# Performance work log

Hardware: AMD Instinct MI355X
Metric: run time of the kernel (lower is better)

## Reference

```python
import jax, jax.numpy as jnp
from jax import lax
import numpy as np

B, NW, L, E, H, V = 8192, 4, 16, 128, 128, 64  # batch, words/example, max chars, emsize, hidden, char vocab


def setup_inputs() -> dict:
    key = jax.random.key(0)
    ks = jax.random.split(key, 13)
    s = 0.05
    return {
        "word_ids": jax.random.randint(ks[0], (B, NW, L), 0, V, dtype=jnp.int32),
        "lengths": jax.random.randint(ks[1], (B, NW), 1, L + 1, dtype=jnp.int32),
        "emb_i": jax.random.normal(ks[2], (V, E), jnp.float32),
        "W_ih": jax.random.normal(ks[3], (4 * H, E), jnp.float32) * s,
        "W_hh": jax.random.normal(ks[4], (4 * H, H), jnp.float32) * s,
        "b_ih": jax.random.normal(ks[5], (4 * H,), jnp.float32) * s,
        "b_hh": jax.random.normal(ks[6], (4 * H,), jnp.float32) * s,
        "conv1_w": jax.random.normal(ks[7], (4, 1, 2, 2), jnp.float32) * 0.5,
        "conv1_b": jax.random.normal(ks[8], (4,), jnp.float32) * 0.1,
        "conv2_w": jax.random.normal(ks[9], (8, 4, 2, 2), jnp.float32) * 0.5,
        "conv2_b": jax.random.normal(ks[10], (8,), jnp.float32) * 0.1,
        "scorer_w": jax.random.normal(ks[11], (1, 2 * 2 * 8), jnp.float32) * 0.2,
        "scorer_b": jax.random.normal(ks[12], (1,), jnp.float32) * 0.1,
    }


def reference(word_ids, lengths, emb_i, W_ih, W_hh, b_ih, b_hh,
              conv1_w, conv1_b, conv2_w, conv2_b, scorer_w, scorer_b):
    Bx, NWx, Lx = word_ids.shape
    Hh = W_hh.shape[1]
    BN = Bx * NWx
    # char embeddings for all words, packed: [L, BN, E]
    xs = emb_i[word_ids.reshape(BN, Lx)].transpose(1, 0, 2)
    # ragged lengths -> per-step update mask [L, BN]
    mask = jnp.arange(Lx, dtype=lengths.dtype)[:, None] < lengths.reshape(-1)[None, :]
    h0 = jnp.zeros((BN, Hh), emb_i.dtype)

    def step(carry, xm):
        h, c = carry
        x_t, m = xm
        gates = x_t @ W_ih.T + b_ih + h @ W_hh.T + b_hh  # torch LSTMCell gate order i,f,g,o
        i, f, g, o = jnp.split(gates, 4, axis=-1)
        i = jax.nn.sigmoid(i); f = jax.nn.sigmoid(f)
        g = jnp.tanh(g); o = jax.nn.sigmoid(o)
        c_new = f * c + i * g
        h_new = o * jnp.tanh(c_new)
        m = m[:, None]
        return (jnp.where(m, h_new, h), jnp.where(m, c_new, c)), None

    (h, c), _ = lax.scan(step, (h0, h0), (xs, mask))
    # Model.encode returns the cell state c
    reps = c.reshape(Bx, NWx, Hh)

    # pairwise cosine similarity matrix [B, NW, NW]
    norms = jnp.sqrt(jnp.sum(reps * reps, axis=-1))
    dots = jnp.einsum('bih,bjh->bij', reps, reps)
    cos = dots / (norms[:, :, None] * norms[:, None, :])

    # tiny 2-layer CNN scorer on the NWxNW matrix (NCHW)
    dn = ('NCHW', 'OIHW', 'NCHW')
    x_img = cos[:, None, :, :]
    out = jax.nn.relu(lax.conv_general_dilated(x_img, conv1_w, (1, 1), 'VALID', dimension_numbers=dn)
                      + conv1_b[None, :, None, None])
    out = jax.nn.relu(lax.conv_general_dilated(out, conv2_w, (1, 1), 'VALID', dimension_numbers=dn)
                      + conv2_b[None, :, None, None])
    flat = out.reshape(Bx, -1)  # channel-major flatten matches torch .view
    score = flat @ scorer_w.T + scorer_b
    return jax.nn.sigmoid(score)  # [B, 1] discriminator prob
```

## Files before the change

### kernel.cpp

```cpp
#include <hip/hip_runtime.h>

#define BSZ    8192
#define NWRD   4
#define SEQL   16
#define HDIM   128
#define NSEQ   (BSZ * NWRD)
#define WGSEQ  32
#define UPB    80
#define BINCAP (UPB * WGSEQ)
#define NUNITS (16 * UPB)
#define HSTRIDE 136

typedef float  f32x4  __attribute__((ext_vector_type(4)));
typedef float  f32x16 __attribute__((ext_vector_type(16)));
typedef __bf16 bf16x8 __attribute__((ext_vector_type(8)));

union AccU { f32x16 v; f32x4 q[4]; float f[16]; };
union HPack { unsigned short s[4]; unsigned long long u64; };

__device__ __forceinline__ unsigned short f2bf(float f) {
    unsigned int u = __builtin_bit_cast(unsigned int, f);
    return (unsigned short)((u + 0x7fff + ((u >> 16) & 1)) >> 16);
}
__device__ __forceinline__ float sigm(float x) {
    return __builtin_amdgcn_rcpf(1.f + __builtin_amdgcn_exp2f(x * -1.44269504f));
}
__device__ __forceinline__ float tanhx(float x) {
    return 1.f - 2.f * __builtin_amdgcn_rcpf(1.f + __builtin_amdgcn_exp2f(x * 2.88539008f));
}

__global__ void prep4(const float* __restrict__ emb, const float* __restrict__ W_ih,
                      const float* __restrict__ b_ih, const float* __restrict__ b_hh,
                      const float* __restrict__ W_hh, const int* __restrict__ lengths,
                      float* __restrict__ P2T, unsigned short* __restrict__ WA,
                      int* __restrict__ perm, int* __restrict__ gh)
{
    __shared__ int lh[16], gbase[16];
    const int blk = blockIdx.x, tid = threadIdx.x;

    if (blk < 128) {
        int idx = blk * 256 + tid;
        int v = idx >> 9, g = (idx >> 7) & 3, j = idx & 127;
        int n = g * 128 + j;
        float s = b_ih[n] + b_hh[n];
        const float* er = emb  + v * 128;
        const float* wr = W_ih + n * 128;
        for (int e = 0; e < 128; e += 4)
            s += er[e]*wr[e] + er[e+1]*wr[e+1] + er[e+2]*wr[e+2] + er[e+3]*wr[e+3];
        P2T[idx] = s;
    } else if (blk < 384) {
        int idx = (blk - 128) * 256 + tid;
        int jj = idx & 7, lane = (idx >> 3) & 63, kc = (idx >> 9) & 7, tt = idx >> 12;
        int wv = tt >> 2, g = tt & 3;
        int n = g * 128 + wv * 32 + (lane & 31);
        int k = kc * 16 + (lane >> 5) * 8 + jj;
        WA[idx] = f2bf(W_hh[n * 128 + k]);
    } else {
        if (tid < 16) lh[tid] = 0;
        __syncthreads();
        int i = (blk - 384) * 256 + tid;
        int b = 16 - lengths[i];
        int rank = atomicAdd(&lh[b], 1);
        __syncthreads();
        if (tid < 16) gbase[tid] = atomicAdd(&gh[tid], lh[tid]);
        __syncthreads();
        perm[b * BINCAP + gbase[b] + rank] = i;
    }
}

__global__ __launch_bounds__(256, 2) void lstm4(
    const int* __restrict__ word_ids, const int* __restrict__ perm,
    const int* __restrict__ gh, const float* __restrict__ P2T,
    const unsigned short* __restrict__ WA, float* __restrict__ c_out)
{
    __shared__ __align__(16) unsigned short hbuf[2][WGSEQ * HSTRIDE];
    __shared__ int words_s[WGSEQ * 17];
    __shared__ int sid_s[WGSEQ];

    const int tid    = threadIdx.x;
    const int wv     = tid >> 6;
    const int lane   = tid & 63;
    const int lane31 = lane & 31;
    const int hl     = lane >> 5;

    const int u    = blockIdx.x;
    const int b    = u / UPB;
    const int widx = u % UPB;
    const int cnt  = gh[b];
    const int ml   = (widx * WGSEQ < cnt) ? (16 - b) : 0;

    bf16x8 afr[4][8];
#pragma unroll
    for (int g = 0; g < 4; ++g)
#pragma unroll
        for (int kc = 0; kc < 8; ++kc)
            afr[g][kc] = *(const bf16x8*)(WA + (((wv * 4 + g) * 8 + kc) * 64 + lane) * 8);

    if (tid < WGSEQ) {
        int slot = widx * WGSEQ + tid;
        sid_s[tid] = (slot < cnt) ? perm[b * BINCAP + slot] : 0;
    }
    for (int i = tid; i < WGSEQ * HSTRIDE; i += 256) ((int*)hbuf)[i] = 0;
    __syncthreads();
    for (int i = tid; i < WGSEQ * SEQL; i += 256)
        words_s[(i >> 4) * 17 + (i & 15)] = word_ids[sid_s[i >> 4] * SEQL + (i & 15)];
    __syncthreads();

    if (ml > 0) {
        f32x4 cq[4] = {{0,0,0,0},{0,0,0,0},{0,0,0,0},{0,0,0,0}};
        const char* P2c  = (const char*)P2T;
        const int pboff  = wv * 128 + hl * 16;
        const int rdo    = lane31 * HSTRIDE;
        const int jbase  = wv * 32 + 4 * hl;

#pragma unroll 1
        for (int t = 0; t < ml; ++t) {
            const unsigned short* __restrict__ hr = hbuf[t & 1];
            unsigned short*       __restrict__ hw = hbuf[(t + 1) & 1];

            const int w = words_s[lane31 * 17 + t];
            const char* pb = P2c + ((size_t)w << 11) + pboff;
            AccU acc[4];
#pragma unroll
            for (int g = 0; g < 4; ++g)
#pragma unroll
                for (int q = 0; q < 4; ++q)
                    acc[g].q[q] = *(const f32x4*)(pb + g * 512 + q * 32);

            bf16x8 bf[8];
#pragma unroll
            for (int kc = 0; kc < 8; ++kc)
                bf[kc] = *(const bf16x8*)(hr + rdo + kc * 16 + hl * 8);

#pragma unroll
            for (int kc = 0; kc < 8; ++kc) {
                const bf16x8 bb = bf[kc];
#pragma unroll
                for (int g = 0; g < 4; ++g)
                    acc[g].v = __builtin_amdgcn_mfma_f32_32x32x16_bf16(afr[g][kc], bb, acc[g].v, 0, 0, 0);
            }

#pragma unroll
            for (int q = 0; q < 4; ++q) {
                HPack hp;
#pragma unroll
                for (int d = 0; d < 4; ++d) {
                    const int r = q * 4 + d;
                    float ig = sigm(acc[0].f[r]);
                    float fg = sigm(acc[1].f[r]);
                    float gg = tanhx(acc[2].f[r]);
                    float og = sigm(acc[3].f[r]);
                    float cn = fg * cq[q][d] + ig * gg;
                    cq[q][d] = cn;
                    hp.s[d] = f2bf(og * tanhx(cn));
                }
                *(unsigned long long*)(hw + rdo + jbase + 8 * q) = hp.u64;
            }
            __syncthreads();
        }

        if (widx * WGSEQ + lane31 < cnt) {
            const int sid = sid_s[lane31];
#pragma unroll
            for (int q = 0; q < 4; ++q)
                *(f32x4*)(c_out + sid * HDIM + jbase + 8 * q) = cq[q];
        }
    }
}

__global__ __launch_bounds__(256) void epilogue(
    const float* __restrict__ c_ws,
    const float* __restrict__ conv1_w, const float* __restrict__ conv1_b,
    const float* __restrict__ conv2_w, const float* __restrict__ conv2_b,
    const float* __restrict__ scorer_w, const float* __restrict__ scorer_b,
    float* __restrict__ out)
{
    __shared__ __align__(16) float reps[8 * NWRD * HDIM];
    __shared__ float gram_s[8 * 16];

    const int tid = threadIdx.x;
    const int b0  = blockIdx.x * 8;

    for (int i = tid; i < 8 * NWRD * HDIM; i += 256)
        reps[i] = c_ws[b0 * NWRD * HDIM + i];
    __syncthreads();

    const int bt  = tid >> 5;
    const int sub = tid & 31;

    float dval = 0.f;
    if (sub < 16) {
        int i = sub >> 2, j = sub & 3;
        const f32x4* ci = (const f32x4*)(reps + (bt * 4 + i) * HDIM);
        const f32x4* cj = (const f32x4*)(reps + (bt * 4 + j) * HDIM);
        f32x4 s4 = {0.f, 0.f, 0.f, 0.f};
        for (int k = 0; k < HDIM / 4; ++k) s4 += ci[k] * cj[k];
        dval = s4.x + s4.y + s4.z + s4.w;
        gram_s[bt * 16 + sub] = dval;
    }
    __syncthreads();
    float cosv = 0.f;
    if (sub < 16) {
        int i = sub >> 2, j = sub & 3;
        float di = gram_s[bt * 16 + i * 4 + i];
        float dj = gram_s[bt * 16 + j * 4 + j];
        cosv = __fdividef(dval, sqrtf(di * dj));
    }
    __syncthreads();
    if (sub < 16) gram_s[bt * 16 + sub] = cosv;
    __syncthreads();

    if (sub == 0) {
        float img[4][4];
#pragma unroll
        for (int i = 0; i < 4; ++i)
#pragma unroll
            for (int j = 0; j < 4; ++j) img[i][j] = gram_s[bt * 16 + i * 4 + j];

        float o1[4][3][3];
#pragma unroll
        for (int ch = 0; ch < 4; ++ch) {
            float w00 = conv1_w[ch*4+0], w01 = conv1_w[ch*4+1];
            float w10 = conv1_w[ch*4+2], w11 = conv1_w[ch*4+3];
            float bb  = conv1_b[ch];
#pragma unroll
            for (int y = 0; y < 3; ++y)
#pragma unroll
                for (int x = 0; x < 3; ++x) {
                    float s = bb + w00*img[y][x]   + w01*img[y][x+1]
                                 + w10*img[y+1][x] + w11*img[y+1][x+1];
                    o1[ch][y][x] = s > 0.f ? s : 0.f;
                }
        }
        float sc = scorer_b[0];
#pragma unroll
        for (int oc = 0; oc < 8; ++oc) {
            float bb = conv2_b[oc];
#pragma unroll
            for (int y = 0; y < 2; ++y)
#pragma unroll
                for (int x = 0; x < 2; ++x) {
                    float s = bb;
#pragma unroll
                    for (int ic = 0; ic < 4; ++ic) {
                        const float* w = conv2_w + oc * 16 + ic * 4;
                        s += w[0]*o1[ic][y][x]   + w[1]*o1[ic][y][x+1]
                           + w[2]*o1[ic][y+1][x] + w[3]*o1[ic][y+1][x+1];
                    }
                    float rl = s > 0.f ? s : 0.f;
                    sc += rl * scorer_w[oc * 4 + y * 2 + x];
                }
        }
        out[blockIdx.x * 8 + bt] = sigm(sc);
    }
}

extern "C" void kernel_launch(void* const* d_in, const int* in_sizes, int n_in,
                              void* d_out, int out_size, void* d_ws, size_t ws_size,
                              hipStream_t stream)
{
    const int*   word_ids = (const int*)d_in[0];
    const int*   lengths  = (const int*)d_in[1];
    const float* emb      = (const float*)d_in[2];
    const float* W_ih     = (const float*)d_in[3];
    const float* W_hh     = (const float*)d_in[4];
    const float* b_ih     = (const float*)d_in[5];
    const float* b_hh     = (const float*)d_in[6];
    const float* conv1_w  = (const float*)d_in[7];
    const float* conv1_b  = (const float*)d_in[8];
    const float* conv2_w  = (const float*)d_in[9];
    const float* conv2_b  = (const float*)d_in[10];
    const float* scorer_w = (const float*)d_in[11];
    const float* scorer_b = (const float*)d_in[12];
    float* out = (float*)d_out;

    char* ws = (char*)d_ws;
    float*          P2T  = (float*)(ws + 0);
    unsigned short* WA   = (unsigned short*)(ws + (128<<10));
    int*            perm = (int*)(ws + (256<<10));
    int*            gh   = (int*)(ws + (416<<10));
    float*          c_ws = (float*)(ws + (512<<10));

    hipMemsetAsync(gh, 0, 16 * sizeof(int), stream);
    prep4   <<<512,   256, 0, stream>>>(emb, W_ih, b_ih, b_hh, W_hh, lengths,
                                        P2T, WA, perm, gh);
    lstm4   <<<NUNITS, 256, 0, stream>>>(word_ids, perm, gh, P2T, WA, c_ws);
    epilogue<<<BSZ / 8, 256, 0, stream>>>(c_ws, conv1_w, conv1_b, conv2_w, conv2_b,
                                          scorer_w, scorer_b, out);
}
```

Measured before the change: 197.0 us.

## Peel first LSTM step, prefetch next-step input gates, skip dead work

The LSTM loop is restructured. Step 0 skips the MFMA because h is zero, so the hbuf zeroing goes away. The next step's precomputed input-gate loads are issued right after each h slice is written, so their latency overlaps the barrier. The last step skips the output gate and the h write. Empty blocks now exit early before loading the weight fragments, bf16 packing uses the hardware v_cvt_pk_bf16_f32 instruction, and the prep dot product is vectorized.

```diff
diff --git a/kernel.cpp b/kernel.cpp
--- a/kernel.cpp
+++ b/kernel.cpp
@@ -16,7 +16,6 @@
 typedef __bf16 bf16x8 __attribute__((ext_vector_type(8)));
 
 union AccU { f32x16 v; f32x4 q[4]; float f[16]; };
-union HPack { unsigned short s[4]; unsigned long long u64; };
 
 __device__ __forceinline__ unsigned short f2bf(float f) {
     unsigned int u = __builtin_bit_cast(unsigned int, f);
@@ -42,12 +41,12 @@
         int idx = blk * 256 + tid;
         int v = idx >> 9, g = (idx >> 7) & 3, j = idx & 127;
         int n = g * 128 + j;
-        float s = b_ih[n] + b_hh[n];
-        const float* er = emb  + v * 128;
-        const float* wr = W_ih + n * 128;
-        for (int e = 0; e < 128; e += 4)
-            s += er[e]*wr[e] + er[e+1]*wr[e+1] + er[e+2]*wr[e+2] + er[e+3]*wr[e+3];
-        P2T[idx] = s;
+        const f32x4* er = (const f32x4*)(emb  + v * 128);
+        const f32x4* wr = (const f32x4*)(W_ih + n * 128);
+        f32x4 s4 = er[0] * wr[0];
+#pragma unroll
+        for (int e = 1; e < 32; ++e) s4 += er[e] * wr[e];
+        P2T[idx] = s4.x + s4.y + s4.z + s4.w + b_ih[n] + b_hh[n];
     } else if (blk < 384) {
         int idx = (blk - 128) * 256 + tid;
         int jj = idx & 7, lane = (idx >> 3) & 63, kc = (idx >> 9) & 7, tt = idx >> 12;
@@ -68,6 +67,64 @@
     }
 }
 
+
+#define GATE_PHASE(T, WRITE)                                                    \
+    {                                                                           \
+        const int wr_ = (WRITE);                                                \
+        unsigned short* hw_ = hbuf[((T) + 1) & 1];                              \
+        int wn_ = 0;                                                            \
+        if (wr_) wn_ = words_s[lane31 * 17 + (T) + 1];                          \
+        const char* pbn_ = P2c + ((size_t)wn_ << 11) + pboff;                   \
+        _Pragma("unroll")                                                       \
+        for (int q = 0; q < 4; ++q) {                                           \
+            float hv_[4];                                                       \
+            _Pragma("unroll")                                                   \
+            for (int d = 0; d < 4; ++d) {                                       \
+                const int r = q * 4 + d;                                        \
+                float ig = sigm(acc[0].f[r]);                                   \
+                float fg = sigm(acc[1].f[r]);                                   \
+                float gg = tanhx(acc[2].f[r]);                                  \
+                float cn = fg * cq[q][d] + ig * gg;                             \
+                cq[q][d] = cn;                                                  \
+                if (wr_) {                                                      \
+                    float og = sigm(acc[3].f[r]);                               \
+                    hv_[d] = og * tanhx(cn);                                    \
+                }                                                               \
+            }                                                                   \
+            if (wr_) {                                                          \
+                unsigned int plo_, phi_;                                        \
+                asm("v_cvt_pk_bf16_f32 %0, %1, %2"                              \
+                    : "=v"(plo_) : "v"(hv_[0]), "v"(hv_[1]));                   \
+                asm("v_cvt_pk_bf16_f32 %0, %1, %2"                              \
+                    : "=v"(phi_) : "v"(hv_[2]), "v"(hv_[3]));                   \
+                unsigned long long pu_ =                                        \
+                    ((unsigned long long)phi_ << 32) | plo_;                    \
+                *(unsigned long long*)(hw_ + rdo + jbase + 8 * q) = pu_;        \
+                             \
+                _Pragma("unroll")                                               \
+                for (int g = 0; g < 4; ++g)                                     \
+                    acc[g].q[q] = *(const f32x4*)(pbn_ + g * 512 + q * 32);     \
+            }                                                                   \
+        }                                                                       \
+    }
+
+#define MFMA_STEP(T)                                                            \
+    {                                                                           \
+        const unsigned short* hr_ = hbuf[(T) & 1];                              \
+        bf16x8 bfv_[8];                                                         \
+        _Pragma("unroll")                                                       \
+        for (int kc = 0; kc < 8; ++kc)                                          \
+            bfv_[kc] = *(const bf16x8*)(hr_ + rdo + kc * 16 + hl * 8);          \
+        _Pragma("unroll")                                                       \
+        for (int kc = 0; kc < 8; ++kc) {                                        \
+            const bf16x8 bb_ = bfv_[kc];                                        \
+            _Pragma("unroll")                                                   \
+            for (int g = 0; g < 4; ++g)                                         \
+                acc[g].v = __builtin_amdgcn_mfma_f32_32x32x16_bf16(             \
+                    afr[g][kc], bb_, acc[g].v, 0, 0, 0);                        \
+        }                                                                       \
+    }
+
 __global__ __launch_bounds__(256, 2) void lstm4(
     const int* __restrict__ word_ids, const int* __restrict__ perm,
     const int* __restrict__ gh, const float* __restrict__ P2T,
@@ -87,84 +144,60 @@
     const int b    = u / UPB;
     const int widx = u % UPB;
     const int cnt  = gh[b];
-    const int ml   = (widx * WGSEQ < cnt) ? (16 - b) : 0;
-
-    bf16x8 afr[4][8];
-#pragma unroll
-    for (int g = 0; g < 4; ++g)
-#pragma unroll
-        for (int kc = 0; kc < 8; ++kc)
-            afr[g][kc] = *(const bf16x8*)(WA + (((wv * 4 + g) * 8 + kc) * 64 + lane) * 8);
+    if (widx * WGSEQ >= cnt) return;
+    const int ml   = 16 - b;
 
     if (tid < WGSEQ) {
         int slot = widx * WGSEQ + tid;
         sid_s[tid] = (slot < cnt) ? perm[b * BINCAP + slot] : 0;
     }
-    for (int i = tid; i < WGSEQ * HSTRIDE; i += 256) ((int*)hbuf)[i] = 0;
     __syncthreads();
     for (int i = tid; i < WGSEQ * SEQL; i += 256)
         words_s[(i >> 4) * 17 + (i & 15)] = word_ids[sid_s[i >> 4] * SEQL + (i & 15)];
     __syncthreads();
 
-    if (ml > 0) {
-        f32x4 cq[4] = {{0,0,0,0},{0,0,0,0},{0,0,0,0},{0,0,0,0}};
-        const char* P2c  = (const char*)P2T;
-        const int pboff  = wv * 128 + hl * 16;
-        const int rdo    = lane31 * HSTRIDE;
-        const int jbase  = wv * 32 + 4 * hl;
-
+    bf16x8 afr[4][8];
+#pragma unroll
+    for (int g = 0; g < 4; ++g)
+#pragma unroll
+        for (int kc = 0; kc < 8; ++kc)
+            afr[g][kc] = *(const bf16x8*)(WA + (((wv * 4 + g) * 8 + kc) * 64 + lane) * 8);
+
+    f32x4 cq[4] = {{0,0,0,0},{0,0,0,0},{0,0,0,0},{0,0,0,0}};
+    const char* P2c  = (const char*)P2T;
+    const int pboff  = wv * 128 + hl * 16;
+    const int rdo    = lane31 * HSTRIDE;
+    const int jbase  = wv * 32 + 4 * hl;
+
+    AccU acc[4];
+    {
+        const int w0 = words_s[lane31 * 17];
+        const char* pb = P2c + ((size_t)w0 << 11) + pboff;
+#pragma unroll
+        for (int g = 0; g < 4; ++g)
+#pragma unroll
+            for (int q = 0; q < 4; ++q)
+                acc[g].q[q] = *(const f32x4*)(pb + g * 512 + q * 32);
+    }
+
+    GATE_PHASE(0, ml > 1);
+    if (ml > 1) {
+        __syncthreads();
 #pragma unroll 1
-        for (int t = 0; t < ml; ++t) {
-            const unsigned short* __restrict__ hr = hbuf[t & 1];
-            unsigned short*       __restrict__ hw = hbuf[(t + 1) & 1];
-
-            const int w = words_s[lane31 * 17 + t];
-            const char* pb = P2c + ((size_t)w << 11) + pboff;
-            AccU acc[4];
-#pragma unroll
-            for (int g = 0; g < 4; ++g)
-#pragma unroll
-                for (int q = 0; q < 4; ++q)
-                    acc[g].q[q] = *(const f32x4*)(pb + g * 512 + q * 32);
-
-            bf16x8 bf[8];
-#pragma unroll
-            for (int kc = 0; kc < 8; ++kc)
-                bf[kc] = *(const bf16x8*)(hr + rdo + kc * 16 + hl * 8);
-
-#pragma unroll
-            for (int kc = 0; kc < 8; ++kc) {
-                const bf16x8 bb = bf[kc];
-#pragma unroll
-                for (int g = 0; g < 4; ++g)
-                    acc[g].v = __builtin_amdgcn_mfma_f32_32x32x16_bf16(afr[g][kc], bb, acc[g].v, 0, 0, 0);
-            }
-
-#pragma unroll
-            for (int q = 0; q < 4; ++q) {
-                HPack hp;
-#pragma unroll
-                for (int d = 0; d < 4; ++d) {
-                    const int r = q * 4 + d;
-                    float ig = sigm(acc[0].f[r]);
-                    float fg = sigm(acc[1].f[r]);
-                    float gg = tanhx(acc[2].f[r]);
-                    float og = sigm(acc[3].f[r]);
-                    float cn = fg * cq[q][d] + ig * gg;
-                    cq[q][d] = cn;
-                    hp.s[d] = f2bf(og * tanhx(cn));
-                }
-                *(unsigned long long*)(hw + rdo + jbase + 8 * q) = hp.u64;
-            }
+        for (int t = 1; t < ml - 1; ++t) {
+            MFMA_STEP(t);
+            GATE_PHASE(t, 1);
             __syncthreads();
         }
-
-        if (widx * WGSEQ + lane31 < cnt) {
-            const int sid = sid_s[lane31];
-#pragma unroll
-            for (int q = 0; q < 4; ++q)
-                *(f32x4*)(c_out + sid * HDIM + jbase + 8 * q) = cq[q];
-        }
+        MFMA_STEP(ml - 1);
+        GATE_PHASE(ml - 1, 0);
+    }
+
+    if (widx * WGSEQ + lane31 < cnt) {
+        const int sid = sid_s[lane31];
+#pragma unroll
+        for (int q = 0; q < 4; ++q)
+            *(f32x4*)(c_out + sid * HDIM + jbase + 8 * q) = cq[q];
     }
 }
 
```

After: 194.0 us. No clear change (-1.5%).

## Stage fp16 input-projection table in LDS and streamline LSTM recurrence step

Applied to the files above, without the earlier changes.

The precomputed embedding×W_ih projection table is now stored in fp16 with a swizzled layout and bulk-copied into LDS per workgroup with global_load_lds, replacing per-step global reads of the fp32 table. Word ids are packed into registers, the h buffer uses an XOR swizzle instead of padding, the first step skips the recurrent MFMA, the last step skips the h computation, and the gate math merges sigmoid/tanh reciprocals. Empty workgroups exit early. This trades a 64KB LDS footprint per block, which may lower occupancy, and fp16 rounding of the gate pre-activations for fewer global loads and less transcendental work.

```diff
diff --git a/kernel.cpp b/kernel.cpp
--- a/kernel.cpp
+++ b/kernel.cpp
@@ -4,19 +4,23 @@
 #define NWRD   4
 #define SEQL   16
 #define HDIM   128
+#define VOCAB  64
 #define NSEQ   (BSZ * NWRD)
 #define WGSEQ  32
 #define UPB    80
 #define BINCAP (UPB * WGSEQ)
 #define NUNITS (16 * UPB)
-#define HSTRIDE 136
-
-typedef float  f32x4  __attribute__((ext_vector_type(4)));
-typedef float  f32x16 __attribute__((ext_vector_type(16)));
-typedef __bf16 bf16x8 __attribute__((ext_vector_type(8)));
+
+#define AS1 __attribute__((address_space(1)))
+#define AS3 __attribute__((address_space(3)))
+
+typedef float    f32x4  __attribute__((ext_vector_type(4)));
+typedef float    f32x16 __attribute__((ext_vector_type(16)));
+typedef __bf16   bf16x8 __attribute__((ext_vector_type(8)));
+typedef _Float16 f16x8  __attribute__((ext_vector_type(8)));
+typedef int      i32x4  __attribute__((ext_vector_type(4)));
 
 union AccU { f32x16 v; f32x4 q[4]; float f[16]; };
-union HPack { unsigned short s[4]; unsigned long long u64; };
 
 __device__ __forceinline__ unsigned short f2bf(float f) {
     unsigned int u = __builtin_bit_cast(unsigned int, f);
@@ -25,14 +29,11 @@
 __device__ __forceinline__ float sigm(float x) {
     return __builtin_amdgcn_rcpf(1.f + __builtin_amdgcn_exp2f(x * -1.44269504f));
 }
-__device__ __forceinline__ float tanhx(float x) {
-    return 1.f - 2.f * __builtin_amdgcn_rcpf(1.f + __builtin_amdgcn_exp2f(x * 2.88539008f));
-}
 
 __global__ void prep4(const float* __restrict__ emb, const float* __restrict__ W_ih,
                       const float* __restrict__ b_ih, const float* __restrict__ b_hh,
                       const float* __restrict__ W_hh, const int* __restrict__ lengths,
-                      float* __restrict__ P2T, unsigned short* __restrict__ WA,
+                      unsigned short* __restrict__ P2H, unsigned short* __restrict__ WA,
                       int* __restrict__ perm, int* __restrict__ gh)
 {
     __shared__ int lh[16], gbase[16];
@@ -42,12 +43,17 @@
         int idx = blk * 256 + tid;
         int v = idx >> 9, g = (idx >> 7) & 3, j = idx & 127;
         int n = g * 128 + j;
-        float s = b_ih[n] + b_hh[n];
-        const float* er = emb  + v * 128;
-        const float* wr = W_ih + n * 128;
-        for (int e = 0; e < 128; e += 4)
-            s += er[e]*wr[e] + er[e+1]*wr[e+1] + er[e+2]*wr[e+2] + er[e+3]*wr[e+3];
-        P2T[idx] = s;
+        const f32x4* er = (const f32x4*)(emb  + v * 128);
+        const f32x4* wr = (const f32x4*)(W_ih + n * 128);
+        f32x4 s4 = er[0] * wr[0];
+#pragma unroll
+        for (int e = 1; e < 32; ++e) s4 += er[e] * wr[e];
+        float s = s4.x + s4.y + s4.z + s4.w + b_ih[n] + b_hh[n];
+        int wv = j >> 5, jr = j & 31;
+        int d = jr & 3, hl = (jr >> 2) & 1, q = jr >> 3;
+        int cc = g * 16 + wv * 4 + hl * 2 + (q >> 1);
+        int F  = v * 512 + ((cc ^ (v & 7)) << 3) + (q & 1) * 4 + d;
+        P2H[F] = __builtin_bit_cast(unsigned short, (_Float16)s);
     } else if (blk < 384) {
         int idx = (blk - 128) * 256 + tid;
         int jj = idx & 7, lane = (idx >> 3) & 63, kc = (idx >> 9) & 7, tt = idx >> 12;
@@ -70,12 +76,11 @@
 
 __global__ __launch_bounds__(256, 2) void lstm4(
     const int* __restrict__ word_ids, const int* __restrict__ perm,
-    const int* __restrict__ gh, const float* __restrict__ P2T,
+    const int* __restrict__ gh, const unsigned short* __restrict__ P2H,
     const unsigned short* __restrict__ WA, float* __restrict__ c_out)
 {
-    __shared__ __align__(16) unsigned short hbuf[2][WGSEQ * HSTRIDE];
-    __shared__ int words_s[WGSEQ * 17];
-    __shared__ int sid_s[WGSEQ];
+    __shared__ __align__(16) unsigned short ptab[VOCAB * 512];
+    __shared__ __align__(16) unsigned short hbuf[2][WGSEQ * 128];
 
     const int tid    = threadIdx.x;
     const int wv     = tid >> 6;
@@ -87,7 +92,20 @@
     const int b    = u / UPB;
     const int widx = u % UPB;
     const int cnt  = gh[b];
-    const int ml   = (widx * WGSEQ < cnt) ? (16 - b) : 0;
+    if (widx * WGSEQ >= cnt) return;
+    const int ml   = 16 - b;
+
+    {
+        const char* src = (const char*)P2H;
+        char*       dst = (char*)ptab;
+#pragma unroll
+        for (int r = 0; r < 16; ++r) {
+            const int off = r * 4096 + wv * 1024;
+            __builtin_amdgcn_global_load_lds(
+                (const AS1 unsigned int*)(src + off + lane * 16),
+                (AS3 unsigned int*)(dst + off), 16, 0, 0);
+        }
+    }
 
     bf16x8 afr[4][8];
 #pragma unroll
@@ -96,75 +114,108 @@
         for (int kc = 0; kc < 8; ++kc)
             afr[g][kc] = *(const bf16x8*)(WA + (((wv * 4 + g) * 8 + kc) * 64 + lane) * 8);
 
-    if (tid < WGSEQ) {
-        int slot = widx * WGSEQ + tid;
-        sid_s[tid] = (slot < cnt) ? perm[b * BINCAP + slot] : 0;
-    }
-    for (int i = tid; i < WGSEQ * HSTRIDE; i += 256) ((int*)hbuf)[i] = 0;
-    __syncthreads();
-    for (int i = tid; i < WGSEQ * SEQL; i += 256)
-        words_s[(i >> 4) * 17 + (i & 15)] = word_ids[sid_s[i >> 4] * SEQL + (i & 15)];
-    __syncthreads();
-
-    if (ml > 0) {
-        f32x4 cq[4] = {{0,0,0,0},{0,0,0,0},{0,0,0,0},{0,0,0,0}};
-        const char* P2c  = (const char*)P2T;
-        const int pboff  = wv * 128 + hl * 16;
-        const int rdo    = lane31 * HSTRIDE;
-        const int jbase  = wv * 32 + 4 * hl;
+    const int slot = widx * WGSEQ + lane31;
+    const int live = slot < cnt;
+    const int sid  = live ? perm[b * BINCAP + slot] : 0;
+    unsigned long long u0, u1;
+    {
+        const i32x4* wp = (const i32x4*)(word_ids + sid * SEQL);
+        i32x4 a = wp[0], b4 = wp[1], c4 = wp[2], d4 = wp[3];
+        unsigned lo0 = (unsigned)(a.x  | (a.y  << 8) | (a.z  << 16) | (a.w  << 24));
+        unsigned hi0 = (unsigned)(b4.x | (b4.y << 8) | (b4.z << 16) | (b4.w << 24));
+        unsigned lo1 = (unsigned)(c4.x | (c4.y << 8) | (c4.z << 16) | (c4.w << 24));
+        unsigned hi1 = (unsigned)(d4.x | (d4.y << 8) | (d4.z << 16) | (d4.w << 24));
+        u0 = ((unsigned long long)hi0 << 32) | lo0;
+        u1 = ((unsigned long long)hi1 << 32) | lo1;
+    }
+    __syncthreads();
+
+    f32x4 cq[4] = {{0,0,0,0},{0,0,0,0},{0,0,0,0},{0,0,0,0}};
+    const int      rdo_b = lane31 * 256;
+    const unsigned xv    = (unsigned)((lane31 & 7) << 4);
+    const int      jbase = wv * 32 + 4 * hl;
+    const int      ccb   = wv * 4 + hl * 2;
 
 #pragma unroll 1
-        for (int t = 0; t < ml; ++t) {
-            const unsigned short* __restrict__ hr = hbuf[t & 1];
-            unsigned short*       __restrict__ hw = hbuf[(t + 1) & 1];
-
-            const int w = words_s[lane31 * 17 + t];
-            const char* pb = P2c + ((size_t)w << 11) + pboff;
-            AccU acc[4];
+    for (int t = 0; t < ml; ++t) {
+        const int w = (int)(u0 & 63);
+        u0 = (u0 >> 8) | (u1 << 56); u1 >>= 8;
+
+        AccU acc[4];
+        {
+            const char*    rowp = (const char*)ptab + (w << 10);
+            const unsigned wx   = (unsigned)((w & 7) << 4);
 #pragma unroll
             for (int g = 0; g < 4; ++g)
 #pragma unroll
-                for (int q = 0; q < 4; ++q)
-                    acc[g].q[q] = *(const f32x4*)(pb + g * 512 + q * 32);
-
-            bf16x8 bf[8];
+                for (int s = 0; s < 2; ++s) {
+                    const unsigned off = ((unsigned)((g * 16 + ccb + s) << 4)) ^ wx;
+                    f16x8 hv = *(const f16x8*)(rowp + off);
+#pragma unroll
+                    for (int k = 0; k < 8; ++k)
+                        acc[g].f[s * 8 + k] = (float)hv[k];
+                }
+        }
+
+        if (t > 0) {
+            const char* hr = (const char*)hbuf[t & 1];
+            bf16x8 bfv[8];
 #pragma unroll
             for (int kc = 0; kc < 8; ++kc)
-                bf[kc] = *(const bf16x8*)(hr + rdo + kc * 16 + hl * 8);
-
+                bfv[kc] = *(const bf16x8*)(hr + rdo_b +
+                              (((unsigned)(kc * 32 + hl * 16)) ^ xv));
 #pragma unroll
             for (int kc = 0; kc < 8; ++kc) {
-                const bf16x8 bb = bf[kc];
+                const bf16x8 bb = bfv[kc];
 #pragma unroll
                 for (int g = 0; g < 4; ++g)
-                    acc[g].v = __builtin_amdgcn_mfma_f32_32x32x16_bf16(afr[g][kc], bb, acc[g].v, 0, 0, 0);
+                    acc[g].v = __builtin_amdgcn_mfma_f32_32x32x16_bf16(
+                        afr[g][kc], bb, acc[g].v, 0, 0, 0);
             }
-
-#pragma unroll
-            for (int q = 0; q < 4; ++q) {
-                HPack hp;
-#pragma unroll
-                for (int d = 0; d < 4; ++d) {
-                    const int r = q * 4 + d;
-                    float ig = sigm(acc[0].f[r]);
-                    float fg = sigm(acc[1].f[r]);
-                    float gg = tanhx(acc[2].f[r]);
-                    float og = sigm(acc[3].f[r]);
-                    float cn = fg * cq[q][d] + ig * gg;
-                    cq[q][d] = cn;
-                    hp.s[d] = f2bf(og * tanhx(cn));
+        }
+
+        const int wr = (t < ml - 1);
+        char* hw = (char*)hbuf[(t + 1) & 1];
+#pragma unroll
+        for (int q = 0; q < 4; ++q) {
+            float hv4[4];
+#pragma unroll
+            for (int d = 0; d < 4; ++d) {
+                const int r = q * 4 + d;
+                float ei = __builtin_amdgcn_exp2f(acc[0].f[r] * -1.44269504f);
+                float ef = __builtin_amdgcn_exp2f(acc[1].f[r] * -1.44269504f);
+                float eg = __builtin_amdgcn_exp2f(acc[2].f[r] *  2.88539008f);
+                float fg  = __builtin_amdgcn_rcpf(1.f + ef);
+                float igg = (eg - 1.f) *
+                            __builtin_amdgcn_rcpf((1.f + ei) * (1.f + eg));
+                float cn = cq[q][d] * fg + igg;
+                cq[q][d] = cn;
+                if (wr) {
+                    float eo = __builtin_amdgcn_exp2f(acc[3].f[r] * -1.44269504f);
+                    float ec = __builtin_amdgcn_exp2f(cn * 2.88539008f);
+                    hv4[d] = (ec - 1.f) *
+                             __builtin_amdgcn_rcpf((1.f + eo) * (1.f + ec));
                 }
-                *(unsigned long long*)(hw + rdo + jbase + 8 * q) = hp.u64;
             }
-            __syncthreads();
-        }
-
-        if (widx * WGSEQ + lane31 < cnt) {
-            const int sid = sid_s[lane31];
-#pragma unroll
-            for (int q = 0; q < 4; ++q)
-                *(f32x4*)(c_out + sid * HDIM + jbase + 8 * q) = cq[q];
-        }
+            if (wr) {
+                unsigned int plo_, phi_;
+                asm("v_cvt_pk_bf16_f32 %0, %1, %2"
+                    : "=v"(plo_) : "v"(hv4[0]), "v"(hv4[1]));
+                asm("v_cvt_pk_bf16_f32 %0, %1, %2"
+                    : "=v"(phi_) : "v"(hv4[2]), "v"(hv4[3]));
+                unsigned long long pu_ =
+                    ((unsigned long long)phi_ << 32) | plo_;
+                *(unsigned long long*)(hw + rdo_b +
+                    (((unsigned)(wv * 64 + q * 16)) ^ xv) + hl * 8) = pu_;
+            }
+        }
+        if (wr) __syncthreads();
+    }
+
+    if (live) {
+#pragma unroll
+        for (int q = 0; q < 4; ++q)
+            *(f32x4*)(c_out + sid * HDIM + jbase + 8 * q) = cq[q];
     }
 }
 
@@ -275,7 +326,7 @@
     float* out = (float*)d_out;
 
     char* ws = (char*)d_ws;
-    float*          P2T  = (float*)(ws + 0);
+    unsigned short* P2H  = (unsigned short*)(ws + 0);
     unsigned short* WA   = (unsigned short*)(ws + (128<<10));
     int*            perm = (int*)(ws + (256<<10));
     int*            gh   = (int*)(ws + (416<<10));
@@ -283,8 +334,8 @@
 
     hipMemsetAsync(gh, 0, 16 * sizeof(int), stream);
     prep4   <<<512,   256, 0, stream>>>(emb, W_ih, b_ih, b_hh, W_hh, lengths,
-                                        P2T, WA, perm, gh);
-    lstm4   <<<NUNITS, 256, 0, stream>>>(word_ids, perm, gh, P2T, WA, c_ws);
+                                        P2H, WA, perm, gh);
+    lstm4   <<<NUNITS, 256, 0, stream>>>(word_ids, perm, gh, P2H, WA, c_ws);
     epilogue<<<BSZ / 8, 256, 0, stream>>>(c_ws, conv1_w, conv1_b, conv2_w, conv2_b,
                                           scorer_w, scorer_b, out);
 }
```

Measured after the change: 172.3 us. -12.5%, faster.
